# Optimization experiments

Hardware: AMD Instinct MI355X
Metric: run time of the kernel (lower is better)

Reference implementation:

```python
import jax, jax.numpy as jnp
import numpy as np

B = 131072   # batch
F = 64       # n_features
G = 8        # number of groups
GS = 8       # group size
NB = 16      # n_basis
O = 64       # out_dim per group
BN_EPS = 1e-5


def setup_inputs() -> dict:
    key = jax.random.key(0)
    k0, k1, k2 = jax.random.split(key, 3)
    x = jax.random.normal(k0, (B, F), dtype=jnp.float32)
    indices = jnp.arange(G * GS, dtype=jnp.int64).reshape(G, GS)  # group_map as array
    centres = jnp.tile(jnp.linspace(-3.0, 3.0, NB, dtype=jnp.float32), (G, 1))  # (G,NB)
    log_widths = jnp.zeros((G, NB), dtype=jnp.float32)
    rbf_weights = jax.random.normal(k1, (G, NB), dtype=jnp.float32) * 0.1
    linear_weight = jnp.ones((G,), dtype=jnp.float32)
    # kaiming_normal fan_in relu: std = sqrt(2 / fan_in)
    proj_w = jax.random.normal(k2, (G, O, GS), dtype=jnp.float32) * np.sqrt(2.0 / GS)
    proj_b = jnp.zeros((G, O), dtype=jnp.float32)
    bn_gamma = jnp.ones((G * O,), dtype=jnp.float32)
    bn_beta = jnp.zeros((G * O,), dtype=jnp.float32)
    return {
        "x": x, "centres": centres, "log_widths": log_widths,
        "rbf_weights": rbf_weights, "linear_weight": linear_weight,
        "proj_w": proj_w, "proj_b": proj_b,
        "bn_gamma": bn_gamma, "bn_beta": bn_beta, "indices": indices,
    }


def reference(x, centres, log_widths, rbf_weights, linear_weight,
              proj_w, proj_b, bn_gamma, bn_beta, indices):
    xg = x[:, indices]                                   # (B,G,GS) gather per group
    sigma = jnp.exp(log_widths) + 1e-6                   # (G,NB)
    diff = (xg[..., None] - centres[None, :, None, :]) / sigma[None, :, None, :]  # (B,G,GS,NB)
    rbf = jnp.exp(-0.5 * diff * diff)
    rbf_out = linear_weight[None, :, None] * xg + jnp.sum(rbf * rbf_weights[None, :, None, :], axis=-1)  # (B,G,GS)
    proj = jnp.einsum('bgs,gos->bgo', rbf_out, proj_w) + proj_b[None]  # (B,G,O)
    out = proj.reshape(B, G * O)
    # BatchNorm1d, training mode (biased batch variance)
    mean = jnp.mean(out, axis=0)
    var = jnp.mean((out - mean) ** 2, axis=0)
    out = (out - mean) * jax.lax.rsqrt(var + BN_EPS) * bn_gamma + bn_beta
    return out
```

## Files before the change

### kernel.cpp

```cpp
#include <hip/hip_runtime.h>


#define B_ROWS 131072
#define NFEAT  64
#define NJ     512
#define NBAS   16
#define BN_EPS 1e-5f

#define MOFF    2048
#define NBUF    16
#define TBL_OFF 8192
#define TBL_N   512
#define TBL_XMIN (-8.0f)
#define TBL_H    (16.0f / TBL_N)
#define TBL_INVH (TBL_N / 16.0f)
#define TBL_BIAS (-TBL_XMIN * TBL_INVH)
#define RBF_OFF 16384

typedef float f32x4 __attribute__((ext_vector_type(4)));
typedef float f32x2 __attribute__((ext_vector_type(2)));

__device__ __forceinline__ float rfl(float v) {
    return __int_as_float(__builtin_amdgcn_readfirstlane(__float_as_int(v)));
}


__global__ __launch_bounds__(512)
void kan_build_table(const float* __restrict__ centres,
                     const float* __restrict__ log_widths,
                     const float* __restrict__ rbf_w,
                     const float* __restrict__ lin_w,
                     float* __restrict__ ws)
{
    const int g = blockIdx.x;

    float cc[NBAS], A[NBAS], w[NBAS];
#pragma unroll
    for (int nb = 0; nb < NBAS; ++nb) {
        cc[nb] = centres[g * NBAS + nb];
        const float is = 1.0f / (__expf(log_widths[g * NBAS + nb]) + 1e-6f);
        A[nb]  = -0.5f * is * is;
        w[nb]  = rbf_w[g * NBAS + nb];
    }
    const float lw = lin_w[g];

    for (int i = threadIdx.x; i < TBL_N; i += 512) {
        float node[2];
#pragma unroll
        for (int e = 0; e < 2; ++e) {
            const float xv = TBL_XMIN + (float)(i + e) * TBL_H;
            float acc = lw * xv;
#pragma unroll
            for (int nb = 0; nb < NBAS; ++nb) {
                const float d = xv - cc[nb];
                acc += w[nb] * __expf(A[nb] * d * d);
            }
            node[e] = acc;
        }
        ws[TBL_OFF + g * (TBL_N * 2) + i * 2]     = node[0];
        ws[TBL_OFF + g * (TBL_N * 2) + i * 2 + 1] = node[1];
    }
}

template <int CACHE>
__global__ __launch_bounds__(512)
void kan_moments4(const float* __restrict__ x,
                  float* __restrict__ ws)
{
    __shared__ f32x2 s_tbl[8][TBL_N];
    __shared__ float s_red[352];

    const int t = threadIdx.x;
    const int l = t & 63;
    const int g = __builtin_amdgcn_readfirstlane(t >> 6);

    {
        const f32x2* src = reinterpret_cast<const f32x2*>(ws + TBL_OFF);
        f32x2* dst = &s_tbl[0][0];
        for (int k = t; k < 8 * TBL_N; k += 512) dst[k] = src[k];
    }
    __syncthreads();

    float S1[8] = {0,0,0,0,0,0,0,0};
    float Mt[36];
#pragma unroll
    for (int k = 0; k < 36; ++k) Mt[k] = 0.0f;

    const int rbase = blockIdx.x * 256 + l;

    const float* xp0 = x + (size_t)rbase * NFEAT + g * 8;
    f32x4 v0 = *reinterpret_cast<const f32x4*>(xp0);
    f32x4 v1 = *reinterpret_cast<const f32x4*>(xp0 + 4);

    for (int it = 0; it < 4; ++it) {
        f32x4 n0, n1;
        if (it + 1 < 4) {
            const float* np = x + (size_t)(rbase + (it + 1) * 64) * NFEAT + g * 8;
            n0 = *reinterpret_cast<const f32x4*>(np);
            n1 = *reinterpret_cast<const f32x4*>(np + 4);
        }

        float r[8];
#pragma unroll
        for (int s = 0; s < 8; ++s) {
            const float xv = (s < 4) ? v0[s] : v1[s - 4];
            float u = fmaf(xv, TBL_INVH, TBL_BIAS);
            u = fminf(fmaxf(u, 0.0f), (float)TBL_N - 1.0005f);
            const float fi = floorf(u);
            const int idx  = (int)fi;
            const float fr = u - fi;
            const f32x2 p  = s_tbl[g][idx];
            r[s] = fmaf(fr, p[1] - p[0], p[0]);
        }

        if (CACHE) {
            float* cp = ws + RBF_OFF + (size_t)(rbase + it * 64) * NFEAT + g * 8;
            f32x4 c0 = {r[0], r[1], r[2], r[3]};
            f32x4 c1 = {r[4], r[5], r[6], r[7]};
            *reinterpret_cast<f32x4*>(cp)     = c0;
            *reinterpret_cast<f32x4*>(cp + 4) = c1;
        }

        int ti = 0;
#pragma unroll
        for (int s = 0; s < 8; ++s) {
            S1[s] += r[s];
#pragma unroll
            for (int sp = s; sp < 8; ++sp) {
                Mt[ti] += r[s] * r[sp];
                ++ti;
            }
        }

        v0 = n0; v1 = n1;
    }

#pragma unroll
    for (int k = 0; k < 36; ++k) {
        float v = Mt[k];
        v += __shfl_xor(v, 1);  v += __shfl_xor(v, 2);  v += __shfl_xor(v, 4);
        v += __shfl_xor(v, 8);  v += __shfl_xor(v, 16); v += __shfl_xor(v, 32);
        Mt[k] = v;
    }
#pragma unroll
    for (int s = 0; s < 8; ++s) {
        float v = S1[s];
        v += __shfl_xor(v, 1);  v += __shfl_xor(v, 2);  v += __shfl_xor(v, 4);
        v += __shfl_xor(v, 8);  v += __shfl_xor(v, 16); v += __shfl_xor(v, 32);
        S1[s] = v;
    }

    if (l == 0) {
#pragma unroll
        for (int k = 0; k < 36; ++k) s_red[g * 44 + k] = Mt[k];
#pragma unroll
        for (int s = 0; s < 8; ++s)  s_red[g * 44 + 36 + s] = S1[s];
    }
    __syncthreads();

    float* mbuf = ws + MOFF + (blockIdx.x & (NBUF - 1)) * 352;
    for (int idx = t; idx < 352; idx += 512)
        atomicAdd(&mbuf[idx], s_red[idx]);
}

__global__ __launch_bounds__(512)
void kan_finalize(const float* __restrict__ proj_w,
                  const float* __restrict__ proj_b,
                  const float* __restrict__ bn_gamma,
                  const float* __restrict__ bn_beta,
                  float* __restrict__ ws)
{
    __shared__ float s_m[352];

    const int t = threadIdx.x;

    for (int idx = t; idx < 352; idx += 512) {
        float v = 0.0f;
#pragma unroll
        for (int b = 0; b < NBUF; ++b) v += ws[MOFF + b * 352 + idx];
        s_m[idx] = v;
    }
    __syncthreads();

    const int j = t;
    const int g = j >> 6;
    const int base = g * 44;

    double pw[8];
#pragma unroll
    for (int s = 0; s < 8; ++s) pw[s] = (double)proj_w[j * 8 + s];
    const double pb = (double)proj_b[j];

    double dotS1 = 0.0;
#pragma unroll
    for (int s = 0; s < 8; ++s)
        dotS1 += pw[s] * (double)s_m[base + 36 + s];

    double q = 0.0;
    int ti = 0;
#pragma unroll
    for (int s = 0; s < 8; ++s) {
#pragma unroll
        for (int sp = s; sp < 8; ++sp) {
            const double m = (double)s_m[base + ti];
            q += (s == sp ? 1.0 : 2.0) * pw[s] * pw[sp] * m;
            ++ti;
        }
    }

    const double Bd    = (double)B_ROWS;
    const double sum   = dotS1 + Bd * pb;
    const double sumsq = q + 2.0 * pb * dotS1 + Bd * pb * pb;
    const double mean  = sum / Bd;
    double var = sumsq / Bd - mean * mean;
    if (var < 0.0) var = 0.0;
    const double sc = (double)bn_gamma[j] / sqrt(var + (double)BN_EPS);
    ws[1024 + j] = (float)sc;
    ws[1536 + j] = (float)((double)bn_beta[j] - mean * sc);
}

__global__ __launch_bounds__(256, 8)
void kan_write_lean(const float* __restrict__ ws,
                    const float* __restrict__ proj_w,
                    const float* __restrict__ proj_b,
                    float* __restrict__ out)
{
    const int l     = threadIdx.x & 63;
    const int W     = (blockIdx.x * 256 + threadIdx.x) >> 6;
    const int half  = W & 1;
    const int wrow  = (W >> 1) * 16;
    const int j0    = half * 256 + 4 * l;
    const int sbase = (j0 >> 6) * 8;
    const float* rbf = ws + RBF_OFF;

    float pw[4][8], sh[4];
#pragma unroll
    for (int f = 0; f < 4; ++f) {
        const int j = j0 + f;
        const float sc = ws[1024 + j];
#pragma unroll
        for (int s = 0; s < 8; ++s) pw[f][s] = proj_w[j * 8 + s] * sc;
        sh[f] = ws[1536 + j] + proj_b[j] * sc;
    }

    for (int i = 0; i < 16; ++i) {
        const int row = wrow + i;
        const float* rp = &rbf[(size_t)row * NFEAT + sbase];
        const f32x4 a0 = *reinterpret_cast<const f32x4*>(rp);
        const f32x4 a1 = *reinterpret_cast<const f32x4*>(rp + 4);

        f32x4 ra;
#pragma unroll
        for (int f = 0; f < 4; ++f)
            ra[f] = a0[0]*pw[f][0] + a0[1]*pw[f][1] + a0[2]*pw[f][2]
                  + a0[3]*pw[f][3] + a1[0]*pw[f][4] + a1[1]*pw[f][5]
                  + a1[2]*pw[f][6] + a1[3]*pw[f][7] + sh[f];

        __builtin_nontemporal_store(ra,
            reinterpret_cast<f32x4*>(&out[(size_t)row * NJ + j0]));
    }
}

__global__ __launch_bounds__(512)
void kan_moments3f(const float* __restrict__ x,
                   const float* __restrict__ centres,
                   const float* __restrict__ log_widths,
                   const float* __restrict__ rbf_w,
                   const float* __restrict__ lin_w,
                   float* __restrict__ ws)
{
    __shared__ float s_red[352];

    const int t = threadIdx.x;
    const int l = t & 63;
    const int g = __builtin_amdgcn_readfirstlane(t >> 6);

    float cc[NBAS], A[NBAS], w[NBAS];
#pragma unroll
    for (int nb = 0; nb < NBAS; ++nb) {
        cc[nb] = centres[g * NBAS + nb];
        const float is = 1.0f / (__expf(log_widths[g * NBAS + nb]) + 1e-6f);
        A[nb]  = rfl(-0.5f * is * is);
        w[nb]  = rbf_w[g * NBAS + nb];
    }
    const float lw = rfl(lin_w[g]);

    float S1[8] = {0,0,0,0,0,0,0,0};
    float Mt[36];
#pragma unroll
    for (int k = 0; k < 36; ++k) Mt[k] = 0.0f;

    const int rbase = blockIdx.x * 256 + l;

    for (int it = 0; it < 4; ++it) {
        const float* xp = x + (size_t)(rbase + it * 64) * NFEAT + g * 8;
        const f32x4 v0 = *reinterpret_cast<const f32x4*>(xp);
        const f32x4 v1 = *reinterpret_cast<const f32x4*>(xp + 4);

        float r[8];
#pragma unroll
        for (int s = 0; s < 8; ++s) {
            const float xv = (s < 4) ? v0[s] : v1[s - 4];
            float acc = lw * xv;
#pragma unroll
            for (int nb = 0; nb < NBAS; ++nb) {
                const float d = xv - cc[nb];
                acc += w[nb] * __expf(A[nb] * d * d);
            }
            r[s] = acc;
        }

        int ti = 0;
#pragma unroll
        for (int s = 0; s < 8; ++s) {
            S1[s] += r[s];
#pragma unroll
            for (int sp = s; sp < 8; ++sp) { Mt[ti] += r[s] * r[sp]; ++ti; }
        }
    }

#pragma unroll
    for (int k = 0; k < 36; ++k) {
        float v = Mt[k];
        v += __shfl_xor(v, 1);  v += __shfl_xor(v, 2);  v += __shfl_xor(v, 4);
        v += __shfl_xor(v, 8);  v += __shfl_xor(v, 16); v += __shfl_xor(v, 32);
        Mt[k] = v;
    }
#pragma unroll
    for (int s = 0; s < 8; ++s) {
        float v = S1[s];
        v += __shfl_xor(v, 1);  v += __shfl_xor(v, 2);  v += __shfl_xor(v, 4);
        v += __shfl_xor(v, 8);  v += __shfl_xor(v, 16); v += __shfl_xor(v, 32);
        S1[s] = v;
    }

    if (l == 0) {
#pragma unroll
        for (int k = 0; k < 36; ++k) s_red[g * 44 + k] = Mt[k];
#pragma unroll
        for (int s = 0; s < 8; ++s)  s_red[g * 44 + 36 + s] = S1[s];
    }
    __syncthreads();

    float* mbuf = ws + MOFF + (blockIdx.x & (NBUF - 1)) * 352;
    for (int idx = t; idx < 352; idx += 512)
        atomicAdd(&mbuf[idx], s_red[idx]);
}

__global__ __launch_bounds__(256)
void kan_write_rc(const float* __restrict__ x,
                  const float* __restrict__ centres,
                  const float* __restrict__ log_widths,
                  const float* __restrict__ rbf_w,
                  const float* __restrict__ lin_w,
                  const float* __restrict__ proj_w,
                  const float* __restrict__ proj_b,
                  const float* __restrict__ ws,
                  float* __restrict__ out)
{
    const int l  = threadIdx.x & 63;
    const int wv = (blockIdx.x * 256 + threadIdx.x) >> 6;
    const int g  = l >> 3;
    const int bl = (l >> 4) * 8;
    const int bh = bl + 32;

    float cc[NBAS], A[NBAS], w[NBAS];
#pragma unroll
    for (int nb = 0; nb < NBAS; ++nb) {
        cc[nb] = centres[g * NBAS + nb];
        const float is = 1.0f / (__expf(log_widths[g * NBAS + nb]) + 1e-6f);
        A[nb]  = -0.5f * is * is;
        w[nb]  = rbf_w[g * NBAS + nb];
    }
    const float lw = lin_w[g];

    float pwl[4][8], pwh[4][8], scl[4], shl[4], sch[4], shh[4];
#pragma unroll
    for (int f = 0; f < 4; ++f) {
        const int jl = 4 * l + f;
        const int jh = 256 + 4 * l + f;
#pragma unroll
        for (int s = 0; s < 8; ++s) {
            pwl[f][s] = proj_w[jl * 8 + s];
            pwh[f][s] = proj_w[jh * 8 + s];
        }
        scl[f] = ws[1024 + jl];
        shl[f] = ws[1536 + jl] + proj_b[jl] * scl[f];
        sch[f] = ws[1024 + jh];
        shh[f] = ws[1536 + jh] + proj_b[jh] * sch[f];
    }

    const int row0 = wv * 16;
    float xa = x[(size_t)row0 * NFEAT + l];
    float xb = x[(size_t)(row0 + 1) * NFEAT + l];

    for (int i = 0; i < 16; i += 2) {
        const int row = row0 + i;
        float na = 0.0f, nb2 = 0.0f;
        if (i + 2 < 16) {
            na  = x[(size_t)(row + 2) * NFEAT + l];
            nb2 = x[(size_t)(row + 3) * NFEAT + l];
        }

        float ra = lw * xa;
        float rb = lw * xb;
#pragma unroll
        for (int nb = 0; nb < NBAS; ++nb) {
            const float da = xa - cc[nb];
            const float db = xb - cc[nb];
            ra += w[nb] * __expf(A[nb] * da * da);
            rb += w[nb] * __expf(A[nb] * db * db);
        }

        float val[8], vah[8], vbl[8], vbh[8];
#pragma unroll
        for (int s = 0; s < 8; ++s) {
            val[s] = __shfl(ra, bl + s);
            vah[s] = __shfl(ra, bh + s);
            vbl[s] = __shfl(rb, bl + s);
            vbh[s] = __shfl(rb, bh + s);
        }

        f32x4 r0, r1, r2, r3;
#pragma unroll
        for (int f = 0; f < 4; ++f) {
            r0[f] = (val[0]*pwl[f][0] + val[1]*pwl[f][1] + val[2]*pwl[f][2]
                   + val[3]*pwl[f][3] + val[4]*pwl[f][4] + val[5]*pwl[f][5]
                   + val[6]*pwl[f][6] + val[7]*pwl[f][7]) * scl[f] + shl[f];
            r1[f] = (vah[0]*pwh[f][0] + vah[1]*pwh[f][1] + vah[2]*pwh[f][2]
                   + vah[3]*pwh[f][3] + vah[4]*pwh[f][4] + vah[5]*pwh[f][5]
                   + vah[6]*pwh[f][6] + vah[7]*pwh[f][7]) * sch[f] + shh[f];
            r2[f] = (vbl[0]*pwl[f][0] + vbl[1]*pwl[f][1] + vbl[2]*pwl[f][2]
                   + vbl[3]*pwl[f][3] + vbl[4]*pwl[f][4] + vbl[5]*pwl[f][5]
                   + vbl[6]*pwl[f][6] + vbl[7]*pwl[f][7]) * scl[f] + shl[f];
            r3[f] = (vbh[0]*pwh[f][0] + vbh[1]*pwh[f][1] + vbh[2]*pwh[f][2]
                   + vbh[3]*pwh[f][3] + vbh[4]*pwh[f][4] + vbh[5]*pwh[f][5]
                   + vbh[6]*pwh[f][6] + vbh[7]*pwh[f][7]) * sch[f] + shh[f];
        }

        float* oa = &out[(size_t)row * NJ];
        float* ob = &out[(size_t)(row + 1) * NJ];
        __builtin_nontemporal_store(r0, reinterpret_cast<f32x4*>(oa + 4 * l));
        __builtin_nontemporal_store(r1, reinterpret_cast<f32x4*>(oa + 256 + 4 * l));
        __builtin_nontemporal_store(r2, reinterpret_cast<f32x4*>(ob + 4 * l));
        __builtin_nontemporal_store(r3, reinterpret_cast<f32x4*>(ob + 256 + 4 * l));

        xa = na;
        xb = nb2;
    }
}

extern "C" void kernel_launch(void* const* d_in, const int* in_sizes, int n_in,
                              void* d_out, int out_size, void* d_ws, size_t ws_size,
                              hipStream_t stream)
{
    const float* x           = (const float*)d_in[0];
    const float* centres     = (const float*)d_in[1];
    const float* log_widths  = (const float*)d_in[2];
    const float* rbf_weights = (const float*)d_in[3];
    const float* linear_w    = (const float*)d_in[4];
    const float* proj_w      = (const float*)d_in[5];
    const float* proj_b      = (const float*)d_in[6];
    const float* bn_gamma    = (const float*)d_in[7];
    const float* bn_beta     = (const float*)d_in[8];

    float* ws  = (float*)d_ws;
    float* out = (float*)d_out;

    const bool cache_ok =
        ws_size >= (size_t)(RBF_OFF + (size_t)B_ROWS * NFEAT) * sizeof(float);

    (void)hipMemsetAsync(ws + 1024, 0, (7680 - 1024) * sizeof(float), stream);

    if (cache_ok) {
        kan_build_table<<<8, 512, 0, stream>>>(centres, log_widths,
                                               rbf_weights, linear_w, ws);
        kan_moments4<1><<<512, 512, 0, stream>>>(x, ws);
        kan_finalize<<<1, 512, 0, stream>>>(proj_w, proj_b, bn_gamma, bn_beta, ws);
        kan_write_lean<<<4096, 256, 0, stream>>>(ws, proj_w, proj_b, out);
    } else {
        kan_moments3f<<<512, 512, 0, stream>>>(x, centres, log_widths,
                                               rbf_weights, linear_w, ws);
        kan_finalize<<<1, 512, 0, stream>>>(proj_w, proj_b, bn_gamma, bn_beta, ws);
        kan_write_rc<<<2048, 256, 0, stream>>>(x, centres, log_widths, rbf_weights,
                                               linear_w, proj_w, proj_b, ws, out);
    }
}
```

Before: 95.55 us.

## Fuse table build and BN finalize into moments kernel via last-block counter

The separate table-build and finalize kernels are removed. Each moments block now builds its own per-group RBF lookup table in shared memory, using 256 intervals stored as a scalar array with padded stride. The last block to finish, detected with an atomic counter, performs the BatchNorm scale/shift finalize. This saves two kernel launches and their gaps, at the cost of redundant table computation in every block and a serialized tail on one block.

```diff
diff --git a/kernel.cpp b/kernel.cpp
--- a/kernel.cpp
+++ b/kernel.cpp
@@ -7,18 +7,19 @@
 #define NBAS   16
 #define BN_EPS 1e-5f
 
+#define CTR     1008
 #define MOFF    2048
 #define NBUF    16
-#define TBL_OFF 8192
-#define TBL_N   512
+#define RBF_OFF 8192
+
+#define TBL_N    256
+#define TBL_STRIDE 260
 #define TBL_XMIN (-8.0f)
 #define TBL_H    (16.0f / TBL_N)
 #define TBL_INVH (TBL_N / 16.0f)
 #define TBL_BIAS (-TBL_XMIN * TBL_INVH)
-#define RBF_OFF 16384
 
 typedef float f32x4 __attribute__((ext_vector_type(4)));
-typedef float f32x2 __attribute__((ext_vector_type(2)));
 
 __device__ __forceinline__ float rfl(float v) {
     return __int_as_float(__builtin_amdgcn_readfirstlane(__float_as_int(v)));
@@ -26,58 +27,50 @@
 
 
 __global__ __launch_bounds__(512)
-void kan_build_table(const float* __restrict__ centres,
-                     const float* __restrict__ log_widths,
-                     const float* __restrict__ rbf_w,
-                     const float* __restrict__ lin_w,
-                     float* __restrict__ ws)
-{
-    const int g = blockIdx.x;
-
-    float cc[NBAS], A[NBAS], w[NBAS];
-#pragma unroll
-    for (int nb = 0; nb < NBAS; ++nb) {
-        cc[nb] = centres[g * NBAS + nb];
-        const float is = 1.0f / (__expf(log_widths[g * NBAS + nb]) + 1e-6f);
-        A[nb]  = -0.5f * is * is;
-        w[nb]  = rbf_w[g * NBAS + nb];
-    }
-    const float lw = lin_w[g];
-
-    for (int i = threadIdx.x; i < TBL_N; i += 512) {
-        float node[2];
-#pragma unroll
-        for (int e = 0; e < 2; ++e) {
-            const float xv = TBL_XMIN + (float)(i + e) * TBL_H;
-            float acc = lw * xv;
-#pragma unroll
-            for (int nb = 0; nb < NBAS; ++nb) {
-                const float d = xv - cc[nb];
-                acc += w[nb] * __expf(A[nb] * d * d);
-            }
-            node[e] = acc;
-        }
-        ws[TBL_OFF + g * (TBL_N * 2) + i * 2]     = node[0];
-        ws[TBL_OFF + g * (TBL_N * 2) + i * 2 + 1] = node[1];
-    }
-}
-
-template <int CACHE>
-__global__ __launch_bounds__(512)
-void kan_moments4(const float* __restrict__ x,
+void kan_moments5(const float* __restrict__ x,
+                  const float* __restrict__ centres,
+                  const float* __restrict__ log_widths,
+                  const float* __restrict__ rbf_w,
+                  const float* __restrict__ lin_w,
+                  const float* __restrict__ proj_w,
+                  const float* __restrict__ proj_b,
+                  const float* __restrict__ bn_gamma,
+                  const float* __restrict__ bn_beta,
                   float* __restrict__ ws)
 {
-    __shared__ f32x2 s_tbl[8][TBL_N];
+    __shared__ float s_tbl[8 * TBL_STRIDE];
     __shared__ float s_red[352];
+    __shared__ int   s_last;
 
     const int t = threadIdx.x;
     const int l = t & 63;
     const int g = __builtin_amdgcn_readfirstlane(t >> 6);
 
     {
-        const f32x2* src = reinterpret_cast<const f32x2*>(ws + TBL_OFF);
-        f32x2* dst = &s_tbl[0][0];
-        for (int k = t; k < 8 * TBL_N; k += 512) dst[k] = src[k];
+        float cc[NBAS], A[NBAS], w[NBAS];
+#pragma unroll
+        for (int nb = 0; nb < NBAS; ++nb) {
+            cc[nb] = centres[g * NBAS + nb];
+            const float is = 1.0f / (__expf(log_widths[g * NBAS + nb]) + 1e-6f);
+            A[nb]  = rfl(-0.5f * is * is);
+            w[nb]  = rbf_w[g * NBAS + nb];
+        }
+        const float lw = rfl(lin_w[g]);
+
+#pragma unroll
+        for (int k = 0; k < 5; ++k) {
+            const int i = l + k * 64;
+            if (i < TBL_N + 1) {
+                const float xv = TBL_XMIN + (float)i * TBL_H;
+                float acc = lw * xv;
+#pragma unroll
+                for (int nb = 0; nb < NBAS; ++nb) {
+                    const float d = xv - cc[nb];
+                    acc += w[nb] * __expf(A[nb] * d * d);
+                }
+                s_tbl[g * TBL_STRIDE + i] = acc;
+            }
+        }
     }
     __syncthreads();
 
@@ -87,6 +80,7 @@
     for (int k = 0; k < 36; ++k) Mt[k] = 0.0f;
 
     const int rbase = blockIdx.x * 256 + l;
+    const float* tb = &s_tbl[g * TBL_STRIDE];
 
     const float* xp0 = x + (size_t)rbase * NFEAT + g * 8;
     f32x4 v0 = *reinterpret_cast<const f32x4*>(xp0);
@@ -105,15 +99,16 @@
         for (int s = 0; s < 8; ++s) {
             const float xv = (s < 4) ? v0[s] : v1[s - 4];
             float u = fmaf(xv, TBL_INVH, TBL_BIAS);
-            u = fminf(fmaxf(u, 0.0f), (float)TBL_N - 1.0005f);
+            u = fminf(fmaxf(u, 0.0f), (float)TBL_N - 0.0005f);
             const float fi = floorf(u);
             const int idx  = (int)fi;
             const float fr = u - fi;
-            const f32x2 p  = s_tbl[g][idx];
-            r[s] = fmaf(fr, p[1] - p[0], p[0]);
-        }
-
-        if (CACHE) {
+            const float t0 = tb[idx];
+            const float t1 = tb[idx + 1];
+            r[s] = fmaf(fr, t1 - t0, t0);
+        }
+
+        {
             float* cp = ws + RBF_OFF + (size_t)(rbase + it * 64) * NFEAT + g * 8;
             f32x4 c0 = {r[0], r[1], r[2], r[3]};
             f32x4 c1 = {r[4], r[5], r[6], r[7]};
@@ -126,10 +121,7 @@
         for (int s = 0; s < 8; ++s) {
             S1[s] += r[s];
 #pragma unroll
-            for (int sp = s; sp < 8; ++sp) {
-                Mt[ti] += r[s] * r[sp];
-                ++ti;
-            }
+            for (int sp = s; sp < 8; ++sp) { Mt[ti] += r[s] * r[sp]; ++ti; }
         }
 
         v0 = n0; v1 = n1;
@@ -161,62 +153,62 @@
     float* mbuf = ws + MOFF + (blockIdx.x & (NBUF - 1)) * 352;
     for (int idx = t; idx < 352; idx += 512)
         atomicAdd(&mbuf[idx], s_red[idx]);
-}
-
-__global__ __launch_bounds__(512)
-void kan_finalize(const float* __restrict__ proj_w,
-                  const float* __restrict__ proj_b,
-                  const float* __restrict__ bn_gamma,
-                  const float* __restrict__ bn_beta,
-                  float* __restrict__ ws)
-{
-    __shared__ float s_m[352];
-
-    const int t = threadIdx.x;
+
+    __syncthreads();
+    if (t == 0) {
+        __threadfence();
+        const unsigned old = atomicAdd((unsigned*)(ws + CTR), 1u);
+        s_last = (old == (unsigned)(gridDim.x - 1)) ? 1 : 0;
+    }
+    __syncthreads();
+    if (!s_last) return;
+    __threadfence();
 
     for (int idx = t; idx < 352; idx += 512) {
         float v = 0.0f;
 #pragma unroll
-        for (int b = 0; b < NBUF; ++b) v += ws[MOFF + b * 352 + idx];
-        s_m[idx] = v;
-    }
-    __syncthreads();
-
-    const int j = t;
-    const int g = j >> 6;
-    const int base = g * 44;
-
-    double pw[8];
-#pragma unroll
-    for (int s = 0; s < 8; ++s) pw[s] = (double)proj_w[j * 8 + s];
-    const double pb = (double)proj_b[j];
-
-    double dotS1 = 0.0;
-#pragma unroll
-    for (int s = 0; s < 8; ++s)
-        dotS1 += pw[s] * (double)s_m[base + 36 + s];
-
-    double q = 0.0;
-    int ti = 0;
-#pragma unroll
-    for (int s = 0; s < 8; ++s) {
-#pragma unroll
-        for (int sp = s; sp < 8; ++sp) {
-            const double m = (double)s_m[base + ti];
-            q += (s == sp ? 1.0 : 2.0) * pw[s] * pw[sp] * m;
-            ++ti;
-        }
-    }
-
-    const double Bd    = (double)B_ROWS;
-    const double sum   = dotS1 + Bd * pb;
-    const double sumsq = q + 2.0 * pb * dotS1 + Bd * pb * pb;
-    const double mean  = sum / Bd;
-    double var = sumsq / Bd - mean * mean;
-    if (var < 0.0) var = 0.0;
-    const double sc = (double)bn_gamma[j] / sqrt(var + (double)BN_EPS);
-    ws[1024 + j] = (float)sc;
-    ws[1536 + j] = (float)((double)bn_beta[j] - mean * sc);
+        for (int b = 0; b < NBUF; ++b)
+            v += atomicAdd(&ws[MOFF + b * 352 + idx], 0.0f);
+        s_red[idx] = v;
+    }
+    __syncthreads();
+
+    {
+        const int j = t;
+        const int base = (j >> 6) * 44;
+
+        double pw[8];
+#pragma unroll
+        for (int s = 0; s < 8; ++s) pw[s] = (double)proj_w[j * 8 + s];
+        const double pb = (double)proj_b[j];
+
+        double dotS1 = 0.0;
+#pragma unroll
+        for (int s = 0; s < 8; ++s)
+            dotS1 += pw[s] * (double)s_red[base + 36 + s];
+
+        double q = 0.0;
+        int ti = 0;
+#pragma unroll
+        for (int s = 0; s < 8; ++s) {
+#pragma unroll
+            for (int sp = s; sp < 8; ++sp) {
+                const double m = (double)s_red[base + ti];
+                q += (s == sp ? 1.0 : 2.0) * pw[s] * pw[sp] * m;
+                ++ti;
+            }
+        }
+
+        const double Bd    = (double)B_ROWS;
+        const double sum   = dotS1 + Bd * pb;
+        const double sumsq = q + 2.0 * pb * dotS1 + Bd * pb * pb;
+        const double mean  = sum / Bd;
+        double var = sumsq / Bd - mean * mean;
+        if (var < 0.0) var = 0.0;
+        const double sc = (double)bn_gamma[j] / sqrt(var + (double)BN_EPS);
+        ws[1024 + j] = (float)sc;
+        ws[1536 + j] = (float)((double)bn_beta[j] - mean * sc);
+    }
 }
 
 __global__ __launch_bounds__(256, 8)
@@ -345,6 +337,61 @@
     float* mbuf = ws + MOFF + (blockIdx.x & (NBUF - 1)) * 352;
     for (int idx = t; idx < 352; idx += 512)
         atomicAdd(&mbuf[idx], s_red[idx]);
+}
+
+__global__ __launch_bounds__(512)
+void kan_finalize(const float* __restrict__ proj_w,
+                  const float* __restrict__ proj_b,
+                  const float* __restrict__ bn_gamma,
+                  const float* __restrict__ bn_beta,
+                  float* __restrict__ ws)
+{
+    __shared__ float s_m[352];
+
+    const int t = threadIdx.x;
+
+    for (int idx = t; idx < 352; idx += 512) {
+        float v = 0.0f;
+#pragma unroll
+        for (int b = 0; b < NBUF; ++b) v += ws[MOFF + b * 352 + idx];
+        s_m[idx] = v;
+    }
+    __syncthreads();
+
+    const int j = t;
+    const int base = (j >> 6) * 44;
+
+    double pw[8];
+#pragma unroll
+    for (int s = 0; s < 8; ++s) pw[s] = (double)proj_w[j * 8 + s];
+    const double pb = (double)proj_b[j];
+
+    double dotS1 = 0.0;
+#pragma unroll
+    for (int s = 0; s < 8; ++s)
+        dotS1 += pw[s] * (double)s_m[base + 36 + s];
+
+    double q = 0.0;
+    int ti = 0;
+#pragma unroll
+    for (int s = 0; s < 8; ++s) {
+#pragma unroll
+        for (int sp = s; sp < 8; ++sp) {
+            const double m = (double)s_m[base + ti];
+            q += (s == sp ? 1.0 : 2.0) * pw[s] * pw[sp] * m;
+            ++ti;
+        }
+    }
+
+    const double Bd    = (double)B_ROWS;
+    const double sum   = dotS1 + Bd * pb;
+    const double sumsq = q + 2.0 * pb * dotS1 + Bd * pb * pb;
+    const double mean  = sum / Bd;
+    double var = sumsq / Bd - mean * mean;
+    if (var < 0.0) var = 0.0;
+    const double sc = (double)bn_gamma[j] / sqrt(var + (double)BN_EPS);
+    ws[1024 + j] = (float)sc;
+    ws[1536 + j] = (float)((double)bn_beta[j] - mean * sc);
 }
 
 __global__ __launch_bounds__(256)
@@ -470,13 +517,13 @@
     const bool cache_ok =
         ws_size >= (size_t)(RBF_OFF + (size_t)B_ROWS * NFEAT) * sizeof(float);
 
-    (void)hipMemsetAsync(ws + 1024, 0, (7680 - 1024) * sizeof(float), stream);
+    (void)hipMemsetAsync(ws + CTR, 0, (7680 - CTR) * sizeof(float), stream);
 
     if (cache_ok) {
-        kan_build_table<<<8, 512, 0, stream>>>(centres, log_widths,
-                                               rbf_weights, linear_w, ws);
-        kan_moments4<1><<<512, 512, 0, stream>>>(x, ws);
-        kan_finalize<<<1, 512, 0, stream>>>(proj_w, proj_b, bn_gamma, bn_beta, ws);
+        kan_moments5<<<512, 512, 0, stream>>>(x, centres, log_widths,
+                                              rbf_weights, linear_w,
+                                              proj_w, proj_b, bn_gamma, bn_beta,
+                                              ws);
         kan_write_lean<<<4096, 256, 0, stream>>>(ws, proj_w, proj_b, out);
     } else {
         kan_moments3f<<<512, 512, 0, stream>>>(x, centres, log_widths,
```

Result: slower. 106.2 us (+11.1%).
